# Optimization experiments

Hardware: AMD Instinct MI355X
Metric: run time of the kernel (lower is better)

Reference implementation:

```python
import jax, jax.numpy as jnp
import numpy as np

B, T, C = 2, 2048, 1024
H, G, D = 16, 4, 64            # n_head, n_group (KV heads), d_head
GROUP = H // G                 # query heads per KV head
WIN, SINK = 512, 4             # sliding window, attention sink
BASE = 10000.0
SCALE = D ** -0.5


def _rope(x, pos):
    """Interleaved RoPE on per-head dim. x: [B, T, h, D]."""
    t = x.shape[1]
    inv_freq = 1.0 / (BASE ** (jnp.arange(0, D, 2, dtype=jnp.float32) / D))  # [D/2]
    theta = (pos + jnp.arange(t, dtype=jnp.float32))[:, None] * inv_freq[None, :]  # [T, D/2]
    cos = jnp.cos(theta)[None, :, None, :]  # [1,T,1,D/2]
    sin = jnp.sin(theta)[None, :, None, :]
    xe, xo = x[..., 0::2], x[..., 1::2]
    re = xe * cos - xo * sin
    ro = xe * sin + xo * cos
    return jnp.stack([re, ro], axis=-1).reshape(x.shape)


def setup_inputs() -> dict:
    key = jax.random.key(0)
    ks = jax.random.split(key, 9)
    s = 0.02
    return {
        "x":  jax.random.normal(ks[0], (B, T, C), jnp.float32),
        "Wq": jax.random.normal(ks[1], (C, H * D), jnp.float32) * s,
        "bq": jnp.zeros((H * D,), jnp.float32),
        "Wk": jax.random.normal(ks[2], (C, G * D), jnp.float32) * s,
        "bk": jnp.zeros((G * D,), jnp.float32),
        "Wv": jax.random.normal(ks[3], (C, G * D), jnp.float32) * s,
        "bv": jnp.zeros((G * D,), jnp.float32),
        "Wo": jax.random.normal(ks[4], (C, C), jnp.float32) * s,
        "bo": jnp.zeros((C,), jnp.float32),
        "pos": 0,
    }


def reference(x, Wq, bq, Wk, bk, Wv, bv, Wo, bo, pos):
    b, t, c = x.shape
    q = (x @ Wq + bq).reshape(b, t, H, D)   # [B,T,H,D]
    k = (x @ Wk + bk).reshape(b, t, G, D)   # [B,T,G,D]
    v = (x @ Wv + bv).reshape(b, t, G, D)
    q = _rope(q, pos)
    k = _rope(k, pos)
    q = q.transpose(0, 2, 1, 3)             # [B,H,T,D]
    k = k.transpose(0, 2, 1, 3)             # [B,G,T,D]
    v = v.transpose(0, 2, 1, 3)
    # GQA: repeat-interleave KV heads to match query heads
    k = jnp.repeat(k, GROUP, axis=1)        # [B,H,T,D]
    v = jnp.repeat(v, GROUP, axis=1)
    # sliding-window + sink causal mask
    i = jnp.arange(t)[:, None]
    j = jnp.arange(t)[None, :]
    mask = (i >= j) & ((j >= i - WIN) | (j < SINK))  # [T,T] bool
    scores = jnp.einsum("bhqd,bhkd->bhqk", q, k) * SCALE
    neg = jnp.finfo(scores.dtype).min
    scores = jnp.where(mask[None, None], scores, neg)
    attn = jax.nn.softmax(scores, axis=-1)
    out = jnp.einsum("bhqk,bhkd->bhqd", attn, v)  # [B,H,T,D]
    out = out.transpose(0, 2, 1, 3).reshape(b, t, c)
    return out @ Wo + bo
```

## Files before the change

### kernel.cpp

```cpp
#include <hip/hip_runtime.h>
#include <stdint.h>
#include <math.h>

typedef short v8s __attribute__((ext_vector_type(8)));
typedef float v4f __attribute__((ext_vector_type(4)));

#define DEVI static __device__ __forceinline__
#define AS1 __attribute__((address_space(1)))
#define AS3 __attribute__((address_space(3)))

static constexpr int Bn = 2;
static constexpr int Tn = 2048;
static constexpr int Hn = 16;
static constexpr int Gn = 4;
static constexpr int NQKV = 1536;
static constexpr int WIN = 512;
static constexpr int SINKN = 4;
#define SCALE_L2E (0.125f * 1.4426950408889634f)

DEVI unsigned short f2bf(float f) {
  unsigned u = __float_as_uint(f);
  u += 0x7fffu + ((u >> 16) & 1u);
  return (unsigned short)(u >> 16);
}
DEVI float bf2f(unsigned short h) { return __uint_as_float(((unsigned)h) << 16); }
DEVI unsigned pack_bf2(float hi, float lo) {
  return __builtin_amdgcn_perm(__float_as_uint(hi), __float_as_uint(lo), 0x07060302u);
}

__global__ __launch_bounds__(256) void k_transpose_all(const float* __restrict__ Wq,
                                                       const float* __restrict__ Wk,
                                                       const float* __restrict__ Wv,
                                                       const float* __restrict__ Wo,
                                                       unsigned short* __restrict__ wt_qkv,
                                                       unsigned short* __restrict__ wt_o,
                                                       const int* __restrict__ posp,
                                                       float2* __restrict__ table,
                                                       const float* __restrict__ bq,
                                                       const float* __restrict__ bk,
                                                       const float* __restrict__ bv,
                                                       float* __restrict__ biasout,
                                                       const float* __restrict__ x,
                                                       unsigned short* __restrict__ xb) {
  int z = blockIdx.z;
  int tx = threadIdx.x, ty = threadIdx.y;
  if (z == 5) {
    int base = (blockIdx.y * 32 + blockIdx.x) * 256 + ty * 32 + tx;
    #pragma unroll
    for (int j = 0; j < 4; ++j) {
      int i = base + j * 262144;
      float4 v = ((const float4*)x)[i];
      ushort4 o;
      o.x = f2bf(v.x); o.y = f2bf(v.y); o.z = f2bf(v.z); o.w = f2bf(v.w);
      ((ushort4*)xb)[i] = o;
    }
    return;
  }
  if (z == 4) {
    int i = (blockIdx.y * 32 + blockIdx.x) * 256 + ty * 32 + tx;
    if (i < Tn * 32) {
      int t = i >> 5, d2 = i & 31;
      float inv = powf(10000.f, -(float)d2 / 32.f);
      float theta = (float)(posp[0] + t) * inv;
      float s, c;
      sincosf(theta, &s, &c);
      table[i] = make_float2(c, s);
    }
    if (i < NQKV)
      biasout[i] = (i < 1024) ? bq[i] * SCALE_L2E : (i < 1280 ? bk[i - 1024] : bv[i - 1280]);
    return;
  }
  const float* W; unsigned short* Wt; int N; float scale = 1.f;
  if (z == 0)      { W = Wq; Wt = wt_qkv;                 N = 1024; scale = SCALE_L2E; }
  else if (z == 1) { W = Wk; Wt = wt_qkv + 1024 * 1024;   N = 256; }
  else if (z == 2) { W = Wv; Wt = wt_qkv + 1280 * 1024;   N = 256; }
  else             { W = Wo; Wt = wt_o;                   N = 1024; }
  int n0 = blockIdx.x * 32, k0 = blockIdx.y * 32;
  if (n0 >= N) return;
  __shared__ float tile[32][33];
  #pragma unroll
  for (int yy = 0; yy < 4; ++yy)
    tile[ty + yy * 8][tx] = W[(size_t)(k0 + ty + yy * 8) * N + n0 + tx];
  __syncthreads();
  #pragma unroll
  for (int yy = 0; yy < 4; ++yy)
    Wt[(size_t)(n0 + ty + yy * 8) * 1024 + k0 + tx] = f2bf(tile[tx][ty + yy * 8] * scale);
}

template <bool F32OUT>
__global__ __launch_bounds__(256) void k_gemm_bt(const unsigned short* __restrict__ A,
                                                 const unsigned short* __restrict__ Bt,
                                                 const float* __restrict__ bias,
                                                 const float2* __restrict__ table,
                                                 float* __restrict__ outF,
                                                 unsigned short* __restrict__ outH,
                                                 unsigned short* __restrict__ vtH,
                                                 int M, int N, int K) {
  __shared__ char As[8192];
  __shared__ char Bs[16384];
  int nx = gridDim.x;
  int nwg = nx * gridDim.y;
  int id = blockIdx.y * nx + blockIdx.x;
  int swz = (id & 7) * (nwg >> 3) + (id >> 3);
  int m0 = (swz / nx) * 64, n0 = (swz % nx) * 128;

  int t = threadIdx.x, lane = t & 63, wave = t >> 6;
  int wm = wave >> 1, wn = wave & 1;
  int l15 = lane & 15, l4 = lane >> 4;
  int l7 = l15 & 7;
  v4f acc[2][4] = {};

  for (int k0 = 0; k0 < K; k0 += 64) {
    __syncthreads();
    #pragma unroll
    for (int p = 0; p < 2; ++p) {
      int cid = p * 256 + t;
      int row = cid >> 3, cc = cid & 7;
      const unsigned short* ga = A + (size_t)(m0 + row) * K + k0 + (cc ^ (row & 7)) * 8;
      __builtin_amdgcn_global_load_lds((const AS1 void*)ga,
                                       (AS3 void*)(As + p * 4096 + wave * 1024), 16, 0, 0);
    }
    #pragma unroll
    for (int p = 0; p < 4; ++p) {
      int cid = p * 256 + t;
      int row = cid >> 3, cc = cid & 7;
      const unsigned short* gb = Bt + (size_t)(n0 + row) * K + k0 + (cc ^ (row & 7)) * 8;
      __builtin_amdgcn_global_load_lds((const AS1 void*)gb,
                                       (AS3 void*)(Bs + p * 4096 + wave * 1024), 16, 0, 0);
    }
    __syncthreads();
    #pragma unroll
    for (int kk = 0; kk < 2; ++kk) {
      v8s af[2], bfr[4];
      #pragma unroll
      for (int mi = 0; mi < 2; ++mi)
        af[mi] = *(const v8s*)(As + (wm * 32 + mi * 16 + l15) * 128 + (((kk * 4 + l4) ^ l7) << 4));
      #pragma unroll
      for (int ni = 0; ni < 4; ++ni)
        bfr[ni] = *(const v8s*)(Bs + (wn * 64 + ni * 16 + l15) * 128 + (((kk * 4 + l4) ^ l7) << 4));
      #pragma unroll
      for (int mi = 0; mi < 2; ++mi)
        #pragma unroll
        for (int ni = 0; ni < 4; ++ni)
          acc[mi][ni] = __builtin_amdgcn_mfma_f32_16x16x32_bf16(af[mi], bfr[ni], acc[mi][ni], 0, 0, 0);
    }
  }

  if (!F32OUT && n0 >= 1280) {
    #pragma unroll
    for (int mi = 0; mi < 2; ++mi) {
      #pragma unroll
      for (int ni = 0; ni < 4; ++ni) {
        int col = n0 + wn * 64 + ni * 16 + l15;
        float bv = bias[col];
        int c2 = col - 1280;
        int gg = c2 >> 6, dd = c2 & 63;
        int row = m0 + wm * 32 + mi * 16 + l4 * 4;
        int bb = row >> 11, tt = row & 2047;
        ushort4 ov;
        ov.x = f2bf(acc[mi][ni][0] + bv);
        ov.y = f2bf(acc[mi][ni][1] + bv);
        ov.z = f2bf(acc[mi][ni][2] + bv);
        ov.w = f2bf(acc[mi][ni][3] + bv);
        *(ushort4*)(vtH + ((size_t)((bb * Gn + gg) * 64 + dd)) * Tn + tt) = ov;
      }
    }
  } else if (!F32OUT) {
    #pragma unroll
    for (int mi = 0; mi < 2; ++mi) {
      #pragma unroll
      for (int ni = 0; ni < 4; ++ni) {
        int col = n0 + wn * 64 + ni * 16 + l15;
        float bv = bias[col];
        int d2 = (col & 63) >> 1;
        bool even = !(col & 1);
        #pragma unroll
        for (int r = 0; r < 4; ++r) {
          int row = m0 + wm * 32 + mi * 16 + l4 * 4 + r;
          int tt = row & 2047;
          float2 cs = table[tt * 32 + d2];
          float v = acc[mi][ni][r] + bv;
          float prt = __shfl_xor(v, 1);
          float ov = even ? (v * cs.x - prt * cs.y) : (prt * cs.y + v * cs.x);
          outH[(size_t)row * N + col] = f2bf(ov);
        }
      }
    }
  } else {
    #pragma unroll
    for (int mi = 0; mi < 2; ++mi) {
      #pragma unroll
      for (int ni = 0; ni < 4; ++ni) {
        int col = n0 + wn * 64 + ni * 16 + l15;
        float bv = bias[col];
        #pragma unroll
        for (int r = 0; r < 4; ++r) {
          int row = m0 + wm * 32 + mi * 16 + l4 * 4 + r;
          outF[(size_t)row * N + col] = acc[mi][ni][r] + bv;
        }
      }
    }
  }
}

__global__ __launch_bounds__(512) void k_attn(const unsigned short* __restrict__ qkv,
                                              const unsigned short* __restrict__ vt,
                                              unsigned short* __restrict__ o) {
  __shared__ char smem[2 * 16384 + 16384];
  int id = blockIdx.x;
  int half = id >> 8, r5 = id & 255;
  int h = r5 >> 4;
  int qtile = half ? (15 - (r5 & 15)) : (r5 & 15);
  int b = half;
  int qt0 = qtile * 128;
  int g = h >> 2;
  int t = threadIdx.x, lane = t & 63, wave = t >> 6;
  int l15 = lane & 15, l4 = lane >> 4;
  int l7 = l15 & 7;
  int qw0 = qt0 + wave * 16;
  char* Pb = smem + 32768 + wave * 2048;

  int jt_end = (qt0 + 127) >> 6;
  int wstart = (qt0 > WIN) ? ((qt0 - WIN) >> 6) : 0;
  int nIt = (wstart > 0) ? (jt_end - wstart + 2) : (jt_end + 1);

  int sr = t >> 3, sc = t & 7;
  int scs = (sc ^ (sr & 7)) << 3;
  const unsigned short* gkb = qkv + (size_t)(b * Tn + sr) * NQKV + 1024 + g * 64 + scs;
  const unsigned short* gvb = vt + ((size_t)((b * Gn + g) * 64 + sr)) * Tn + scs;

  auto stageKV = [&](int buf, int j0) {
    __builtin_amdgcn_global_load_lds((const AS1 void*)(gkb + (size_t)j0 * NQKV),
                                     (AS3 void*)(smem + buf * 16384 + wave * 1024), 16, 0, 0);
    __builtin_amdgcn_global_load_lds((const AS1 void*)(gvb + j0),
                                     (AS3 void*)(smem + buf * 16384 + 8192 + wave * 1024), 16, 0, 0);
  };

  auto jt_of = [&](int it) { return (wstart > 0) ? (it == 0 ? 0 : wstart + it - 1) : it; };

  stageKV(0, jt_of(0) << 6);

  v8s Qf[2];
  #pragma unroll
  for (int hf = 0; hf < 2; ++hf)
    Qf[hf] = *(const v8s*)(qkv + (size_t)(b * Tn + qw0 + l15) * NQKV + h * 64 + hf * 32 + l4 * 8);

  float m = -INFINITY, lsm = 0.f;
  v4f accO[4] = {};

  __syncthreads();

  for (int it = 0; it < nIt; ++it) {
    int cur = it & 1;
    if (it + 1 < nIt) stageKV(cur ^ 1, jt_of(it + 1) << 6);
    int j0 = jt_of(it) << 6;

    bool skip = (j0 > qw0 + 15) || ((j0 + 63 < qw0 - WIN) && (j0 >= SINKN));
    if (!skip) {
      const char* Kb = smem + cur * 16384;
      const char* Vb = Kb + 8192;
      v4f s[4];
      __builtin_amdgcn_s_setprio(1);
      #pragma unroll
      for (int kb = 0; kb < 4; ++kb) {
        int r = kb * 16 + l15;
        v8s kf0 = *(const v8s*)(Kb + r * 128 + ((l4 ^ (r & 7)) << 4));
        v8s kf1 = *(const v8s*)(Kb + r * 128 + (((4 + l4) ^ (r & 7)) << 4));
        v4f z = {};
        z = __builtin_amdgcn_mfma_f32_16x16x32_bf16(kf0, Qf[0], z, 0, 0, 0);
        s[kb] = __builtin_amdgcn_mfma_f32_16x16x32_bf16(kf1, Qf[1], z, 0, 0, 0);
      }
      __builtin_amdgcn_s_setprio(0);
      bool needMask = !((j0 + 63 <= qw0) && (j0 >= qw0 + 15 - WIN));
      if (needMask) {
        #pragma unroll
        for (int kb = 0; kb < 4; ++kb)
          #pragma unroll
          for (int r = 0; r < 4; ++r) {
            int j = j0 + kb * 16 + l4 * 4 + r;
            int qg = qw0 + l15;
            bool valid = (j <= qg) && ((j >= qg - WIN) || (j < SINKN));
            s[kb][r] = valid ? s[kb][r] : -1e30f;
          }
      }
      float mt = -1e30f;
      #pragma unroll
      for (int kb = 0; kb < 4; ++kb)
        #pragma unroll
        for (int r = 0; r < 4; ++r) mt = fmaxf(mt, s[kb][r]);
      mt = fmaxf(mt, __shfl_xor(mt, 16));
      mt = fmaxf(mt, __shfl_xor(mt, 32));
      if (!__all(mt <= m + 8.f)) {
        float mnew = fmaxf(m, mt);
        float alpha = exp2f(m - mnew);
        lsm *= alpha;
        #pragma unroll
        for (int db = 0; db < 4; ++db) {
          accO[db][0] *= alpha; accO[db][1] *= alpha;
          accO[db][2] *= alpha; accO[db][3] *= alpha;
        }
        m = mnew;
      }
      float lsum = 0.f;
      #pragma unroll
      for (int kb = 0; kb < 4; ++kb) {
        float p0 = exp2f(s[kb][0] - m);
        float p1 = exp2f(s[kb][1] - m);
        float p2 = exp2f(s[kb][2] - m);
        float p3 = exp2f(s[kb][3] - m);
        lsum += (p0 + p1) + (p2 + p3);
        unsigned lo = pack_bf2(p1, p0);
        unsigned hi = pack_bf2(p3, p2);
        unsigned long long w = ((unsigned long long)hi << 32) | lo;
        *(unsigned long long*)(Pb + l15 * 128 + ((kb * 32 + l4 * 8) ^ (l7 << 4))) = w;
      }
      lsum += __shfl_xor(lsum, 16);
      lsum += __shfl_xor(lsum, 32);
      lsm += lsum;
      asm volatile("s_waitcnt lgkmcnt(0)" ::: "memory");
      __builtin_amdgcn_sched_barrier(0);

      __builtin_amdgcn_s_setprio(1);
      #pragma unroll
      for (int kc = 0; kc < 2; ++kc) {
        v8s pfrag = *(const v8s*)(Pb + l15 * 128 + ((kc * 64 + l4 * 16) ^ (l7 << 4)));
        #pragma unroll
        for (int db = 0; db < 4; ++db) {
          int d = db * 16 + l15;
          v8s vf = *(const v8s*)(Vb + d * 128 + (((kc * 4 + l4) ^ (d & 7)) << 4));
          accO[db] = __builtin_amdgcn_mfma_f32_16x16x32_bf16(vf, pfrag, accO[db], 0, 0, 0);
        }
      }
      __builtin_amdgcn_s_setprio(0);
    }
    __syncthreads();
  }

  float inv = 1.f / lsm;
  size_t orow = (size_t)(b * Tn + qw0 + l15) * 1024 + h * 64;
  #pragma unroll
  for (int db = 0; db < 4; ++db) {
    int d0 = db * 16 + l4 * 4;
    ushort4 ov;
    ov.x = f2bf(accO[db][0] * inv);
    ov.y = f2bf(accO[db][1] * inv);
    ov.z = f2bf(accO[db][2] * inv);
    ov.w = f2bf(accO[db][3] * inv);
    *(ushort4*)(o + orow + d0) = ov;
  }
}

extern "C" void kernel_launch(void* const* d_in, const int* in_sizes, int n_in,
                              void* d_out, int out_size, void* d_ws, size_t ws_size,
                              hipStream_t stream) {
  const float* x  = (const float*)d_in[0];
  const float* Wq = (const float*)d_in[1];
  const float* bq = (const float*)d_in[2];
  const float* Wk = (const float*)d_in[3];
  const float* bk = (const float*)d_in[4];
  const float* Wv = (const float*)d_in[5];
  const float* bv = (const float*)d_in[6];
  const float* Wo = (const float*)d_in[7];
  const float* bo = (const float*)d_in[8];
  const int*   pos = (const int*)d_in[9];
  float* out = (float*)d_out;

  char* ws = (char*)d_ws;
  unsigned short* xb      = (unsigned short*)(ws);
  unsigned short* wt_qkv  = (unsigned short*)(ws + 8388608);
  unsigned short* wt_o    = (unsigned short*)(ws + 11534336);
  float*          bias_q  = (float*)(ws + 13631488);
  float2*         table   = (float2*)(ws + 13637632);
  unsigned short* qkvb    = (unsigned short*)(ws + 14161920);
  unsigned short* vt      = (unsigned short*)(ws + 26744832);
  unsigned short* attno   = xb;

  k_transpose_all<<<dim3(32, 32, 6), dim3(32, 8), 0, stream>>>(Wq, Wk, Wv, Wo, wt_qkv, wt_o,
                                                               pos, table, bq, bk, bv, bias_q,
                                                               x, xb);
  k_gemm_bt<false><<<dim3(12, 64), 256, 0, stream>>>(xb, wt_qkv, bias_q, table, nullptr, qkvb, vt,
                                                     4096, NQKV, 1024);
  k_attn<<<512, 512, 0, stream>>>(qkvb, vt, attno);
  k_gemm_bt<true><<<dim3(8, 64), 256, 0, stream>>>(attno, wt_o, bo, nullptr, out, nullptr, nullptr,
                                                   4096, 1024, 1024);
}
```

Measured before the change: 77.42 us.

## Use 128-wide KV tiles and handle sink keys in a separate pre-pass

```diff
diff --git a/kernel.cpp b/kernel.cpp
--- a/kernel.cpp
+++ b/kernel.cpp
@@ -203,10 +203,10 @@
   }
 }
 
-__global__ __launch_bounds__(512) void k_attn(const unsigned short* __restrict__ qkv,
-                                              const unsigned short* __restrict__ vt,
-                                              unsigned short* __restrict__ o) {
-  __shared__ char smem[2 * 16384 + 16384];
+__global__ __launch_bounds__(512, 4) void k_attn(const unsigned short* __restrict__ qkv,
+                                                 const unsigned short* __restrict__ vt,
+                                                 unsigned short* __restrict__ o) {
+  __shared__ char smem[2 * 32768 + 16384];
   int id = blockIdx.x;
   int half = id >> 8, r5 = id & 255;
   int h = r5 >> 4;
@@ -218,27 +218,38 @@
   int l15 = lane & 15, l4 = lane >> 4;
   int l7 = l15 & 7;
   int qw0 = qt0 + wave * 16;
-  char* Pb = smem + 32768 + wave * 2048;
-
-  int jt_end = (qt0 + 127) >> 6;
-  int wstart = (qt0 > WIN) ? ((qt0 - WIN) >> 6) : 0;
-  int nIt = (wstart > 0) ? (jt_end - wstart + 2) : (jt_end + 1);
-
-  int sr = t >> 3, sc = t & 7;
-  int scs = (sc ^ (sr & 7)) << 3;
-  const unsigned short* gkb = qkv + (size_t)(b * Tn + sr) * NQKV + 1024 + g * 64 + scs;
-  const unsigned short* gvb = vt + ((size_t)((b * Gn + g) * 64 + sr)) * Tn + scs;
+  char* Pb = smem + 65536 + wave * 2048;
+
+  int jt_end = (qt0 + 127) >> 7;
+  int wstart = (qt0 > WIN) ? ((qt0 - WIN) >> 7) : 0;
+  int nIt = jt_end - wstart + 1;
+  bool sinkPre = (wstart > 0);
+
+  const unsigned short* gk0 = qkv + (size_t)(b * Tn) * NQKV + 1024 + g * 64;
+  const unsigned short* gv0 = vt + (size_t)((b * Gn + g) * 64) * Tn;
 
   auto stageKV = [&](int buf, int j0) {
-    __builtin_amdgcn_global_load_lds((const AS1 void*)(gkb + (size_t)j0 * NQKV),
-                                     (AS3 void*)(smem + buf * 16384 + wave * 1024), 16, 0, 0);
-    __builtin_amdgcn_global_load_lds((const AS1 void*)(gvb + j0),
-                                     (AS3 void*)(smem + buf * 16384 + 8192 + wave * 1024), 16, 0, 0);
+    #pragma unroll
+    for (int p = 0; p < 2; ++p) {
+      int cid = p * 512 + t;
+      int sr = cid >> 3, sc = cid & 7;
+      const unsigned short* ga = gk0 + (size_t)(j0 + sr) * NQKV + ((sc ^ (sr & 7)) << 3);
+      __builtin_amdgcn_global_load_lds((const AS1 void*)ga,
+                                       (AS3 void*)(smem + buf * 32768 + p * 8192 + wave * 1024),
+                                       16, 0, 0);
+    }
+    #pragma unroll
+    for (int p = 0; p < 2; ++p) {
+      int cid = p * 512 + t;
+      int vr = cid >> 4, vc = cid & 15;
+      const unsigned short* gb = gv0 + (size_t)vr * Tn + j0 + ((vc ^ (vr & 15)) << 3);
+      __builtin_amdgcn_global_load_lds((const AS1 void*)gb,
+                                       (AS3 void*)(smem + buf * 32768 + 16384 + p * 8192 + wave * 1024),
+                                       16, 0, 0);
+    }
   };
 
-  auto jt_of = [&](int it) { return (wstart > 0) ? (it == 0 ? 0 : wstart + it - 1) : it; };
-
-  stageKV(0, jt_of(0) << 6);
+  stageKV(0, wstart << 7);
 
   v8s Qf[2];
   #pragma unroll
@@ -248,21 +259,59 @@
   float m = -INFINITY, lsm = 0.f;
   v4f accO[4] = {};
 
+  if (sinkPre) {
+    const unsigned short* kr = gk0 + (size_t)l15 * NQKV + l4 * 8;
+    v8s kf0 = *(const v8s*)(kr);
+    v8s kf1 = *(const v8s*)(kr + 32);
+    v4f z = {};
+    z = __builtin_amdgcn_mfma_f32_16x16x32_bf16(kf0, Qf[0], z, 0, 0, 0);
+    z = __builtin_amdgcn_mfma_f32_16x16x32_bf16(kf1, Qf[1], z, 0, 0, 0);
+    float mt = -1e30f;
+    float pv4[4];
+    #pragma unroll
+    for (int r = 0; r < 4; ++r) {
+      float sv = (l4 == 0) ? z[r] : -1e30f;
+      pv4[r] = sv;
+      mt = fmaxf(mt, sv);
+    }
+    mt = fmaxf(mt, __shfl_xor(mt, 16));
+    mt = fmaxf(mt, __shfl_xor(mt, 32));
+    m = mt;
+    float p0 = exp2f(pv4[0] - m), p1 = exp2f(pv4[1] - m);
+    float p2 = exp2f(pv4[2] - m), p3 = exp2f(pv4[3] - m);
+    float lsum = (p0 + p1) + (p2 + p3);
+    unsigned long long w = ((unsigned long long)pack_bf2(p3, p2) << 32) | pack_bf2(p1, p0);
+    *(unsigned long long*)(Pb + l15 * 128 + ((l4 * 8) ^ (l7 << 4))) = w;
+    *(unsigned long long*)(Pb + l15 * 128 + ((32 + l4 * 8) ^ (l7 << 4))) = 0ull;
+    lsum += __shfl_xor(lsum, 16);
+    lsum += __shfl_xor(lsum, 32);
+    lsm = lsum;
+    asm volatile("s_waitcnt lgkmcnt(0)" ::: "memory");
+    __builtin_amdgcn_sched_barrier(0);
+    v8s pfrag = *(const v8s*)(Pb + l15 * 128 + ((l4 * 16) ^ (l7 << 4)));
+    #pragma unroll
+    for (int db = 0; db < 4; ++db) {
+      int d = db * 16 + l15;
+      v8s vf = *(const v8s*)(gv0 + (size_t)d * Tn + l4 * 8);
+      accO[db] = __builtin_amdgcn_mfma_f32_16x16x32_bf16(vf, pfrag, accO[db], 0, 0, 0);
+    }
+  }
+
   __syncthreads();
 
   for (int it = 0; it < nIt; ++it) {
     int cur = it & 1;
-    if (it + 1 < nIt) stageKV(cur ^ 1, jt_of(it + 1) << 6);
-    int j0 = jt_of(it) << 6;
-
-    bool skip = (j0 > qw0 + 15) || ((j0 + 63 < qw0 - WIN) && (j0 >= SINKN));
+    if (it + 1 < nIt) stageKV(cur ^ 1, (wstart + it + 1) << 7);
+    int j0 = (wstart + it) << 7;
+
+    bool skip = (j0 > qw0 + 15) || ((j0 + 127 < qw0 - WIN) && (j0 >= SINKN));
     if (!skip) {
-      const char* Kb = smem + cur * 16384;
-      const char* Vb = Kb + 8192;
-      v4f s[4];
+      const char* Kb = smem + cur * 32768;
+      const char* Vb = Kb + 16384;
+      v4f s[8];
       __builtin_amdgcn_s_setprio(1);
       #pragma unroll
-      for (int kb = 0; kb < 4; ++kb) {
+      for (int kb = 0; kb < 8; ++kb) {
         int r = kb * 16 + l15;
         v8s kf0 = *(const v8s*)(Kb + r * 128 + ((l4 ^ (r & 7)) << 4));
         v8s kf1 = *(const v8s*)(Kb + r * 128 + (((4 + l4) ^ (r & 7)) << 4));
@@ -271,10 +320,10 @@
         s[kb] = __builtin_amdgcn_mfma_f32_16x16x32_bf16(kf1, Qf[1], z, 0, 0, 0);
       }
       __builtin_amdgcn_s_setprio(0);
-      bool needMask = !((j0 + 63 <= qw0) && (j0 >= qw0 + 15 - WIN));
+      bool needMask = !((j0 + 127 <= qw0) && (j0 >= qw0 + 15 - WIN));
       if (needMask) {
         #pragma unroll
-        for (int kb = 0; kb < 4; ++kb)
+        for (int kb = 0; kb < 8; ++kb)
           #pragma unroll
           for (int r = 0; r < 4; ++r) {
             int j = j0 + kb * 16 + l4 * 4 + r;
@@ -285,7 +334,7 @@
       }
       float mt = -1e30f;
       #pragma unroll
-      for (int kb = 0; kb < 4; ++kb)
+      for (int kb = 0; kb < 8; ++kb)
         #pragma unroll
         for (int r = 0; r < 4; ++r) mt = fmaxf(mt, s[kb][r]);
       mt = fmaxf(mt, __shfl_xor(mt, 16));
@@ -302,24 +351,28 @@
         m = mnew;
       }
       float lsum = 0.f;
-      #pragma unroll
-      for (int kb = 0; kb < 4; ++kb) {
+      unsigned pk2[8][2];
+      #pragma unroll
+      for (int kb = 0; kb < 8; ++kb) {
         float p0 = exp2f(s[kb][0] - m);
         float p1 = exp2f(s[kb][1] - m);
         float p2 = exp2f(s[kb][2] - m);
         float p3 = exp2f(s[kb][3] - m);
         lsum += (p0 + p1) + (p2 + p3);
-        unsigned lo = pack_bf2(p1, p0);
-        unsigned hi = pack_bf2(p3, p2);
-        unsigned long long w = ((unsigned long long)hi << 32) | lo;
-        *(unsigned long long*)(Pb + l15 * 128 + ((kb * 32 + l4 * 8) ^ (l7 << 4))) = w;
+        pk2[kb][0] = pack_bf2(p1, p0);
+        pk2[kb][1] = pack_bf2(p3, p2);
       }
       lsum += __shfl_xor(lsum, 16);
       lsum += __shfl_xor(lsum, 32);
       lsm += lsum;
+
+      #pragma unroll
+      for (int kb = 0; kb < 4; ++kb) {
+        unsigned long long w = ((unsigned long long)pk2[kb][1] << 32) | pk2[kb][0];
+        *(unsigned long long*)(Pb + l15 * 128 + ((kb * 32 + l4 * 8) ^ (l7 << 4))) = w;
+      }
       asm volatile("s_waitcnt lgkmcnt(0)" ::: "memory");
       __builtin_amdgcn_sched_barrier(0);
-
       __builtin_amdgcn_s_setprio(1);
       #pragma unroll
       for (int kc = 0; kc < 2; ++kc) {
@@ -327,7 +380,27 @@
         #pragma unroll
         for (int db = 0; db < 4; ++db) {
           int d = db * 16 + l15;
-          v8s vf = *(const v8s*)(Vb + d * 128 + (((kc * 4 + l4) ^ (d & 7)) << 4));
+          v8s vf = *(const v8s*)(Vb + d * 256 + (((kc * 4 + l4) ^ l15) << 4));
+          accO[db] = __builtin_amdgcn_mfma_f32_16x16x32_bf16(vf, pfrag, accO[db], 0, 0, 0);
+        }
+      }
+      __builtin_amdgcn_s_setprio(0);
+      __builtin_amdgcn_sched_barrier(0);
+      #pragma unroll
+      for (int kb = 4; kb < 8; ++kb) {
+        unsigned long long w = ((unsigned long long)pk2[kb][1] << 32) | pk2[kb][0];
+        *(unsigned long long*)(Pb + l15 * 128 + (((kb - 4) * 32 + l4 * 8) ^ (l7 << 4))) = w;
+      }
+      asm volatile("s_waitcnt lgkmcnt(0)" ::: "memory");
+      __builtin_amdgcn_sched_barrier(0);
+      __builtin_amdgcn_s_setprio(1);
+      #pragma unroll
+      for (int kc = 0; kc < 2; ++kc) {
+        v8s pfrag = *(const v8s*)(Pb + l15 * 128 + ((kc * 64 + l4 * 16) ^ (l7 << 4)));
+        #pragma unroll
+        for (int db = 0; db < 4; ++db) {
+          int d = db * 16 + l15;
+          v8s vf = *(const v8s*)(Vb + d * 256 + (((8 + kc * 4 + l4) ^ l15) << 4));
           accO[db] = __builtin_amdgcn_mfma_f32_16x16x32_bf16(vf, pfrag, accO[db], 0, 0, 0);
         }
       }
```

Measured after the change: 78.56 us. Within noise of the previous version (+1.5%).
